# Kernel optimization log

Hardware: AMD Instinct MI355X
Metric: run time of the kernel (lower is better)

Reference implementation:

```python
import jax, jax.numpy as jnp
import numpy as np

H, F, O, T = 2048, 2048, 2048, 4096  # hidden, feature, output, seq_len


def setup_inputs() -> dict:
    key = jax.random.key(0)
    kx, kf, ki, kc, ko, ky = jax.random.split(key, 6)
    xav = lambda k, shp: jax.random.uniform(k, shp, jnp.float32, -1.0, 1.0) * np.sqrt(6.0 / (shp[0] + shp[1]))
    return {
        "X": jax.random.normal(kx, (T, F), jnp.float32),
        "wf": xav(kf, (H, H + F)), "bf": jnp.zeros((H,), jnp.float32),
        "wi": xav(ki, (H, H + F)), "bi": jnp.zeros((H,), jnp.float32),
        "wc": xav(kc, (H, H + F)), "bc": jnp.zeros((H,), jnp.float32),
        "wo": xav(ko, (H, H + F)), "bo": jnp.zeros((H,), jnp.float32),
        "wy": xav(ky, (O, H)), "by": jnp.zeros((O,), jnp.float32),
    }


def reference(X, wf, bf, wi, bi, wc, bc, wo, bo, wy, by):
    h = wf.shape[0]
    # Fuse the four gate GEMVs into one (same math as four separate matmuls).
    W4 = jnp.concatenate([wf, wi, wc, wo], axis=0)   # (4H, H+F)
    b4 = jnp.concatenate([bf, bi, bc, bo], axis=0)   # (4H,)

    def step(carry, x_t):
        hs, cs = carry
        z = W4 @ jnp.concatenate([hs, x_t]) + b4      # (4H,)
        f = jax.nn.sigmoid(z[:h])
        i = jax.nn.sigmoid(z[h:2 * h])
        g = jnp.tanh(z[2 * h:3 * h])
        o = jax.nn.sigmoid(z[3 * h:])
        cs = f * cs + i * g
        hs = o * jnp.tanh(cs)
        return (hs, cs), None

    init = (jnp.zeros((h,), X.dtype), jnp.zeros((h,), X.dtype))
    (h_T, _), _ = jax.lax.scan(step, init, X)
    # Original returns only the final timestep's projection.
    return wy @ h_T + by
```

## Files before the change

kernel.cpp:

```cpp
#include <hip/hip_runtime.h>
#include <hip/hip_fp16.h>

typedef _Float16 h8 __attribute__((ext_vector_type(8)));
typedef _Float16 h2 __attribute__((ext_vector_type(2)));
typedef float    f4 __attribute__((ext_vector_type(4)));
typedef unsigned int u32;
typedef u32 u32x4 __attribute__((ext_vector_type(4)));

#define HDIM 2048
#define FDIM 2048
#define TSEQ 4096
#define NR   8192

__device__ __forceinline__ float sigmoidf_(float x) { return 1.0f / (1.0f + __expf(-x)); }
__device__ __forceinline__ float tanhf_(float x)    { return 1.0f - 2.0f / (1.0f + __expf(2.0f * x)); }

__device__ __forceinline__ int swz(int g) { return (g & ~15) | ((g ^ (g >> 4)) & 15); }

__global__ __launch_bounds__(256) void gemm_zx(
    const float* __restrict__ X,
    const float* __restrict__ wfp, const float* __restrict__ wip,
    const float* __restrict__ wcp, const float* __restrict__ wop,
    _Float16* __restrict__ Zx)
{
    __shared__ __align__(16) _Float16 As[128 * 32];
    __shared__ __align__(16) _Float16 Bs[128 * 32];
    const int tid  = threadIdx.x;
    const int lane = tid & 63;
    const int wv   = tid >> 6;
    const int bm   = blockIdx.x & 31;
    const int bn   = blockIdx.x >> 5;
    const int m0 = bm * 128, n0 = bn * 128;
    const int g = n0 >> 11;
    const float* wsrc = (g == 0) ? wfp : (g == 1) ? wip : (g == 2) ? wcp : wop;
    const int nr0 = n0 & 2047;

    f4 acc[4][4];
    #pragma unroll
    for (int i = 0; i < 4; ++i)
        #pragma unroll
        for (int j = 0; j < 4; ++j) acc[i][j] = (f4){0.f, 0.f, 0.f, 0.f};

    const int wm = (wv >> 1) * 64, wn = (wv & 1) * 64;
    const int fr = lane & 15, kg = lane >> 4;

    for (int k0 = 0; k0 < FDIM; k0 += 32) {
        __syncthreads();
        #pragma unroll
        for (int r = 0; r < 2; ++r) {
            const int row = r * 64 + (tid >> 2);
            const int col = (tid & 3) * 8;
            const float* ax = &X[(size_t)(m0 + row) * FDIM + k0 + col];
            f4 a0 = *(const f4*)ax, a1 = *(const f4*)(ax + 4);
            h8 av = { (_Float16)a0[0], (_Float16)a0[1], (_Float16)a0[2], (_Float16)a0[3],
                      (_Float16)a1[0], (_Float16)a1[1], (_Float16)a1[2], (_Float16)a1[3] };
            *(h8*)&As[row * 32 + col] = av;
            const float* bx = &wsrc[(size_t)(nr0 + row) * 4096 + 2048 + k0 + col];
            f4 b0 = *(const f4*)bx, b1 = *(const f4*)(bx + 4);
            h8 bv = { (_Float16)b0[0], (_Float16)b0[1], (_Float16)b0[2], (_Float16)b0[3],
                      (_Float16)b1[0], (_Float16)b1[1], (_Float16)b1[2], (_Float16)b1[3] };
            *(h8*)&Bs[row * 32 + col] = bv;
        }
        __syncthreads();
        h8 af[4], bf[4];
        #pragma unroll
        for (int i = 0; i < 4; ++i) af[i] = *(const h8*)&As[(wm + i * 16 + fr) * 32 + kg * 8];
        #pragma unroll
        for (int j = 0; j < 4; ++j) bf[j] = *(const h8*)&Bs[(wn + j * 16 + fr) * 32 + kg * 8];
        #pragma unroll
        for (int i = 0; i < 4; ++i)
            #pragma unroll
            for (int j = 0; j < 4; ++j)
                acc[i][j] = __builtin_amdgcn_mfma_f32_16x16x32_f16(af[i], bf[j], acc[i][j], 0, 0, 0);
    }
    #pragma unroll
    for (int i = 0; i < 4; ++i)
        #pragma unroll
        for (int j = 0; j < 4; ++j)
            #pragma unroll
            for (int q = 0; q < 4; ++q) {
                const int row = m0 + wm + i * 16 + (lane >> 4) * 4 + q;
                const int col = n0 + wn + j * 16 + (lane & 15);
                Zx[(size_t)row * NR + col] = (_Float16)acc[i][j][q];
            }
}

__global__ __launch_bounds__(256, 1) void lstm_rec(
    const float* __restrict__ wfp, const float* __restrict__ wip,
    const float* __restrict__ wcp, const float* __restrict__ wop,
    const float* __restrict__ bfv, const float* __restrict__ biv,
    const float* __restrict__ bcv, const float* __restrict__ bov,
    const _Float16* __restrict__ Zx,
    u32* __restrict__ hword,
    float* __restrict__ hfin)
{
    __shared__ __align__(16) u32 stage[HDIM];

    const int tid = threadIdx.x;
    const int w   = blockIdx.x;
    const int rg  = tid >> 5, cc = tid & 31;

    h8 wreg[4][8];
    #pragma unroll
    for (int q = 0; q < 4; ++q) {
        const float* src = ((q == 0) ? wfp : (q == 1) ? wip : (q == 2) ? wcp : wop)
                           + (size_t)(8 * w + rg) * 4096 + cc * 64;
        #pragma unroll
        for (int i = 0; i < 8; ++i) {
            f4 a0 = *(const f4*)(src + i * 8);
            f4 a1 = *(const f4*)(src + i * 8 + 4);
            wreg[q][i] = (h8){ (_Float16)a0[0], (_Float16)a0[1], (_Float16)a0[2], (_Float16)a0[3],
                               (_Float16)a1[0], (_Float16)a1[1], (_Float16)a1[2], (_Float16)a1[3] };
        }
    }
    float bias0 = 0.f, bias1 = 0.f, bias2 = 0.f, bias3 = 0.f;
    float c_reg = 0.f;
    if (cc == 0) {
        bias0 = bfv[8 * w + rg]; bias1 = biv[8 * w + rg];
        bias2 = bcv[8 * w + rg]; bias3 = bov[8 * w + rg];
    }
    const _Float16* zxp = Zx + 8 * w + rg;

    #pragma unroll 1
    for (int t = 0; t < TSEQ; ++t) {
        float zx0 = 0.f, zx1 = 0.f, zx2 = 0.f, zx3 = 0.f;
        if (cc == 0) {
            const _Float16* zp = zxp + (size_t)t * NR;
            zx0 = (float)zp[0];    zx1 = (float)zp[2048];
            zx2 = (float)zp[4096]; zx3 = (float)zp[6144];
        }

        const u32 texp = (u32)t << 16;
        const size_t slotbase = (size_t)(t & 1) * HDIM;

        if (tid < 64) {
            const u32* sp = hword + slotbase + (size_t)tid * 32;
            u32 s0, s1, s2, s3;
            for (;;) {
                asm volatile(
                    "global_load_dword %0, %4, off sc0 sc1\n\t"
                    "global_load_dword %1, %4, off offset:32 sc0 sc1\n\t"
                    "global_load_dword %2, %4, off offset:64 sc0 sc1\n\t"
                    "global_load_dword %3, %4, off offset:96 sc0 sc1\n\t"
                    "s_waitcnt vmcnt(0)"
                    : "=&v"(s0), "=&v"(s1), "=&v"(s2), "=&v"(s3)
                    : "v"(sp) : "memory");
                const u32 bad = ((s0 ^ texp) | (s1 ^ texp) | (s2 ^ texp) | (s3 ^ texp))
                                & 0xFFFF0000u;
                if (!bad) break;
            }
        }
        __syncthreads();

        const u32* p = hword + slotbase + (size_t)tid * 8;
        u32x4 A, B;
        for (;;) {
            asm volatile(
                "global_load_dwordx4 %0, %2, off sc0 sc1\n\t"
                "global_load_dwordx4 %1, %2, off offset:16 sc0 sc1\n\t"
                "s_waitcnt vmcnt(0)"
                : "=&v"(A), "=&v"(B) : "v"(p) : "memory");
            const u32 bad = ((A.x ^ texp) | (A.y ^ texp) | (A.z ^ texp) | (A.w ^ texp) |
                             (B.x ^ texp) | (B.y ^ texp) | (B.z ^ texp) | (B.w ^ texp))
                            & 0xFFFF0000u;
            if (!bad) break;
            __builtin_amdgcn_s_sleep(1);
        }
        *(u32x4*)&stage[swz(tid * 2) * 4]     = A;
        *(u32x4*)&stage[swz(tid * 2 + 1) * 4] = B;
        __syncthreads();

        float acc[4] = {0.f, 0.f, 0.f, 0.f};
        #pragma unroll
        for (int i = 0; i < 8; ++i) {
            u32x4 ga = *(const u32x4*)&stage[swz(cc * 16 + 2 * i) * 4];
            u32x4 gb = *(const u32x4*)&stage[swz(cc * 16 + 2 * i + 1) * 4];
            const h2 h0  = __builtin_bit_cast(h2, (u32)((ga.x & 0xffffu) | (ga.y << 16)));
            const h2 h1  = __builtin_bit_cast(h2, (u32)((ga.z & 0xffffu) | (ga.w << 16)));
            const h2 h2v = __builtin_bit_cast(h2, (u32)((gb.x & 0xffffu) | (gb.y << 16)));
            const h2 h3  = __builtin_bit_cast(h2, (u32)((gb.z & 0xffffu) | (gb.w << 16)));
            #pragma unroll
            for (int q = 0; q < 4; ++q) {
                const h8 wv8 = wreg[q][i];
                acc[q] = __builtin_amdgcn_fdot2((h2){wv8[0], wv8[1]}, h0,  acc[q], false);
                acc[q] = __builtin_amdgcn_fdot2((h2){wv8[2], wv8[3]}, h1,  acc[q], false);
                acc[q] = __builtin_amdgcn_fdot2((h2){wv8[4], wv8[5]}, h2v, acc[q], false);
                acc[q] = __builtin_amdgcn_fdot2((h2){wv8[6], wv8[7]}, h3,  acc[q], false);
            }
        }
        #pragma unroll
        for (int m = 16; m >= 1; m >>= 1) {
            #pragma unroll
            for (int q = 0; q < 4; ++q) acc[q] += __shfl_xor(acc[q], m, 64);
        }

        if (cc == 0) {
            const float f  = sigmoidf_(acc[0] + zx0 + bias0);
            const float i_ = sigmoidf_(acc[1] + zx1 + bias1);
            const float g_ = tanhf_(acc[2] + zx2 + bias2);
            const float o  = sigmoidf_(acc[3] + zx3 + bias3);
            const float cn = f * c_reg + i_ * g_;
            c_reg = cn;
            const float hn = o * tanhf_(cn);
            const unsigned short hb =
                __builtin_bit_cast(unsigned short, (_Float16)hn);
            const u32 word = ((u32)(t + 1) << 16) | (u32)hb;
            u32* op = hword + (size_t)((t + 1) & 1) * HDIM + 8 * w + rg;
            asm volatile("global_atomic_swap %0, %1, off sc1"
                         :: "v"(op), "v"(word) : "memory");
            if (t == TSEQ - 1) hfin[8 * w + rg] = hn;
        }
    }
}

__global__ __launch_bounds__(256) void proj(
    const float* __restrict__ wy, const float* __restrict__ byv,
    const float* __restrict__ hfin, float* __restrict__ y)
{
    const int row = blockIdx.x;
    const float* wr = wy + (size_t)row * HDIM;
    float s = 0.f;
    for (int k = threadIdx.x * 4; k < HDIM; k += 256 * 4) {
        f4 wv = *(const f4*)&wr[k];
        f4 hv = *(const f4*)&hfin[k];
        s = fmaf(wv[0], hv[0], fmaf(wv[1], hv[1], fmaf(wv[2], hv[2], fmaf(wv[3], hv[3], s))));
    }
    #pragma unroll
    for (int m = 32; m >= 1; m >>= 1) s += __shfl_xor(s, m, 64);
    __shared__ float red[4];
    if ((threadIdx.x & 63) == 0) red[threadIdx.x >> 6] = s;
    __syncthreads();
    if (threadIdx.x == 0) y[row] = red[0] + red[1] + red[2] + red[3] + byv[row];
}

extern "C" void kernel_launch(void* const* d_in, const int* in_sizes, int n_in,
                              void* d_out, int out_size, void* d_ws, size_t ws_size,
                              hipStream_t stream)
{
    (void)in_sizes; (void)n_in; (void)out_size;
    const float* X   = (const float*)d_in[0];
    const float* wfp = (const float*)d_in[1];
    const float* bfv = (const float*)d_in[2];
    const float* wip = (const float*)d_in[3];
    const float* biv = (const float*)d_in[4];
    const float* wcp = (const float*)d_in[5];
    const float* bcv = (const float*)d_in[6];
    const float* wop = (const float*)d_in[7];
    const float* bov = (const float*)d_in[8];
    const float* wy  = (const float*)d_in[9];
    const float* byv = (const float*)d_in[10];
    float* y = (float*)d_out;

    char* ws = (char*)d_ws;
    const size_t need = ((size_t)64 << 20) + ((size_t)64 << 10);
    if (ws_size < need) return;

    _Float16* Zx  = (_Float16*)ws;
    u32* hword    = (u32*)(ws + ((size_t)64 << 20));
    float* hfin   = (float*)(ws + ((size_t)64 << 20) + (16 << 10));

    (void)hipMemsetAsync(hword, 0, 2 * HDIM * sizeof(u32), stream);
    gemm_zx<<<dim3(2048), dim3(256), 0, stream>>>(X, wfp, wip, wcp, wop, Zx);
    lstm_rec<<<dim3(256), dim3(256), 0, stream>>>(wfp, wip, wcp, wop,
                                                  bfv, biv, bcv, bov,
                                                  Zx, hword, hfin);
    proj<<<dim3(2048), dim3(256), 0, stream>>>(wy, byv, hfin, y);
}
```

Baseline: 10.04 ms.

## Move next-step hidden-state fetch into wave 0 and drop one barrier per step

Restructures the per-timestep exchange of the recurrent hidden state. Wave 0 now polls for the next step's h vector at the end of each step and loads all 2048 halves into shared staging (128 bytes per lane). Previously every thread polled and loaded its slice after a barrier, so each step now needs one __syncthreads instead of two and issues far fewer polling loads. In exchange, a single wave serializes 8 wide loads on the critical path. Safety against overwriting the staging buffer relies on wave 0 not finishing its wait until every other wave has already published its h value.

```diff
diff --git a/kernel.cpp b/kernel.cpp
--- a/kernel.cpp
+++ b/kernel.cpp
@@ -121,54 +121,19 @@
     }
     const _Float16* zxp = Zx + 8 * w + rg;
 
+    *(u32x4*)&stage[swz(tid * 2) * 4]     = (u32x4){0, 0, 0, 0};
+    *(u32x4*)&stage[swz(tid * 2 + 1) * 4] = (u32x4){0, 0, 0, 0};
+
     #pragma unroll 1
     for (int t = 0; t < TSEQ; ++t) {
+        __syncthreads();
+
         float zx0 = 0.f, zx1 = 0.f, zx2 = 0.f, zx3 = 0.f;
         if (cc == 0) {
             const _Float16* zp = zxp + (size_t)t * NR;
             zx0 = (float)zp[0];    zx1 = (float)zp[2048];
             zx2 = (float)zp[4096]; zx3 = (float)zp[6144];
         }
-
-        const u32 texp = (u32)t << 16;
-        const size_t slotbase = (size_t)(t & 1) * HDIM;
-
-        if (tid < 64) {
-            const u32* sp = hword + slotbase + (size_t)tid * 32;
-            u32 s0, s1, s2, s3;
-            for (;;) {
-                asm volatile(
-                    "global_load_dword %0, %4, off sc0 sc1\n\t"
-                    "global_load_dword %1, %4, off offset:32 sc0 sc1\n\t"
-                    "global_load_dword %2, %4, off offset:64 sc0 sc1\n\t"
-                    "global_load_dword %3, %4, off offset:96 sc0 sc1\n\t"
-                    "s_waitcnt vmcnt(0)"
-                    : "=&v"(s0), "=&v"(s1), "=&v"(s2), "=&v"(s3)
-                    : "v"(sp) : "memory");
-                const u32 bad = ((s0 ^ texp) | (s1 ^ texp) | (s2 ^ texp) | (s3 ^ texp))
-                                & 0xFFFF0000u;
-                if (!bad) break;
-            }
-        }
-        __syncthreads();
-
-        const u32* p = hword + slotbase + (size_t)tid * 8;
-        u32x4 A, B;
-        for (;;) {
-            asm volatile(
-                "global_load_dwordx4 %0, %2, off sc0 sc1\n\t"
-                "global_load_dwordx4 %1, %2, off offset:16 sc0 sc1\n\t"
-                "s_waitcnt vmcnt(0)"
-                : "=&v"(A), "=&v"(B) : "v"(p) : "memory");
-            const u32 bad = ((A.x ^ texp) | (A.y ^ texp) | (A.z ^ texp) | (A.w ^ texp) |
-                             (B.x ^ texp) | (B.y ^ texp) | (B.z ^ texp) | (B.w ^ texp))
-                            & 0xFFFF0000u;
-            if (!bad) break;
-            __builtin_amdgcn_s_sleep(1);
-        }
-        *(u32x4*)&stage[swz(tid * 2) * 4]     = A;
-        *(u32x4*)&stage[swz(tid * 2 + 1) * 4] = B;
-        __syncthreads();
 
         float acc[4] = {0.f, 0.f, 0.f, 0.f};
         #pragma unroll
@@ -210,6 +175,60 @@
                          :: "v"(op), "v"(word) : "memory");
             if (t == TSEQ - 1) hfin[8 * w + rg] = hn;
         }
+
+        if (tid < 64 && t + 1 < TSEQ) {
+            const u32 nexp = (u32)(t + 1) << 16;
+            const size_t nslot = (size_t)((t + 1) & 1) * HDIM;
+            const u32* sp = hword + nslot + (size_t)tid * 32;
+            u32 s0, s1, s2, s3;
+            for (;;) {
+                asm volatile(
+                    "global_load_dword %0, %4, off sc0 sc1\n\t"
+                    "global_load_dword %1, %4, off offset:32 sc0 sc1\n\t"
+                    "global_load_dword %2, %4, off offset:64 sc0 sc1\n\t"
+                    "global_load_dword %3, %4, off offset:96 sc0 sc1\n\t"
+                    "s_waitcnt vmcnt(0)"
+                    : "=&v"(s0), "=&v"(s1), "=&v"(s2), "=&v"(s3)
+                    : "v"(sp) : "memory");
+                const u32 bad = ((s0 ^ nexp) | (s1 ^ nexp) | (s2 ^ nexp) | (s3 ^ nexp))
+                                & 0xFFFF0000u;
+                if (!bad) break;
+            }
+            u32x4 F0, F1, F2, F3, F4, F5, F6, F7;
+            for (;;) {
+                asm volatile(
+                    "global_load_dwordx4 %0, %8, off sc0 sc1\n\t"
+                    "global_load_dwordx4 %1, %8, off offset:16 sc0 sc1\n\t"
+                    "global_load_dwordx4 %2, %8, off offset:32 sc0 sc1\n\t"
+                    "global_load_dwordx4 %3, %8, off offset:48 sc0 sc1\n\t"
+                    "global_load_dwordx4 %4, %8, off offset:64 sc0 sc1\n\t"
+                    "global_load_dwordx4 %5, %8, off offset:80 sc0 sc1\n\t"
+                    "global_load_dwordx4 %6, %8, off offset:96 sc0 sc1\n\t"
+                    "global_load_dwordx4 %7, %8, off offset:112 sc0 sc1\n\t"
+                    "s_waitcnt vmcnt(0)"
+                    : "=&v"(F0), "=&v"(F1), "=&v"(F2), "=&v"(F3),
+                      "=&v"(F4), "=&v"(F5), "=&v"(F6), "=&v"(F7)
+                    : "v"(sp) : "memory");
+                u32 bad = (F0.x ^ nexp) | (F0.y ^ nexp) | (F0.z ^ nexp) | (F0.w ^ nexp);
+                bad |= (F1.x ^ nexp) | (F1.y ^ nexp) | (F1.z ^ nexp) | (F1.w ^ nexp);
+                bad |= (F2.x ^ nexp) | (F2.y ^ nexp) | (F2.z ^ nexp) | (F2.w ^ nexp);
+                bad |= (F3.x ^ nexp) | (F3.y ^ nexp) | (F3.z ^ nexp) | (F3.w ^ nexp);
+                bad |= (F4.x ^ nexp) | (F4.y ^ nexp) | (F4.z ^ nexp) | (F4.w ^ nexp);
+                bad |= (F5.x ^ nexp) | (F5.y ^ nexp) | (F5.z ^ nexp) | (F5.w ^ nexp);
+                bad |= (F6.x ^ nexp) | (F6.y ^ nexp) | (F6.z ^ nexp) | (F6.w ^ nexp);
+                bad |= (F7.x ^ nexp) | (F7.y ^ nexp) | (F7.z ^ nexp) | (F7.w ^ nexp);
+                if (!(bad & 0xFFFF0000u)) break;
+                __builtin_amdgcn_s_sleep(1);
+            }
+            *(u32x4*)&stage[swz(tid * 8 + 0) * 4] = F0;
+            *(u32x4*)&stage[swz(tid * 8 + 1) * 4] = F1;
+            *(u32x4*)&stage[swz(tid * 8 + 2) * 4] = F2;
+            *(u32x4*)&stage[swz(tid * 8 + 3) * 4] = F3;
+            *(u32x4*)&stage[swz(tid * 8 + 4) * 4] = F4;
+            *(u32x4*)&stage[swz(tid * 8 + 5) * 4] = F5;
+            *(u32x4*)&stage[swz(tid * 8 + 6) * 4] = F6;
+            *(u32x4*)&stage[swz(tid * 8 + 7) * 4] = F7;
+        }
     }
 }
 
```

Measured after the change: 22.56 ms. 125% more time.
